# Performance work log

Measured on AMD Instinct MI355X. Metric: run time of the kernel, lower is better.

## Reference

```python
import jax, jax.numpy as jnp
import numpy as np

N, E = 40000, 640000
IN, HID, OUT = 128, 128, 128


def _lin(key, fan_in, fan_out):
    bound = 1.0 / np.sqrt(fan_in)
    kw, kb = jax.random.split(key)
    W = jax.random.uniform(kw, (fan_in, fan_out), jnp.float32, -bound, bound)
    b = jax.random.uniform(kb, (fan_out,), jnp.float32, -bound, bound)
    return W, b


def setup_inputs() -> dict:
    key = jax.random.key(0)
    ks = jax.random.split(key, 10)
    node_feat = jax.random.normal(ks[0], (N, IN), jnp.float32)
    coord_feat = jax.random.normal(ks[1], (N, 3), jnp.float32)
    src = jax.random.randint(ks[2], (E,), 0, N, jnp.int32)
    dst = jax.random.randint(ks[3], (E,), 0, N, jnp.int32)
    # edge_mlp: Linear(2*IN+1 -> HID), SiLU, Linear(HID -> HID), SiLU
    We1, be1 = _lin(ks[4], 2 * IN + 1, HID)
    We2, be2 = _lin(ks[5], HID, HID)
    # node_mlp: Linear(IN+HID -> HID), SiLU, Linear(HID -> OUT)
    Wn1, bn1 = _lin(ks[6], IN + HID, HID)
    Wn2, bn2 = _lin(ks[7], HID, OUT)
    # coord_mlp: Linear(HID -> HID), SiLU, Linear(HID -> 1, bias=False)
    Wc1, bc1 = _lin(ks[8], HID, HID)
    Wc2, _ = _lin(ks[9], HID, 1)
    return {"node_feat": node_feat, "coord_feat": coord_feat, "src": src, "dst": dst,
            "We1": We1, "be1": be1, "We2": We2, "be2": be2,
            "Wn1": Wn1, "bn1": bn1, "Wn2": Wn2, "bn2": bn2,
            "Wc1": Wc1, "bc1": bc1, "Wc2": Wc2}


def reference(node_feat, coord_feat, src, dst,
              We1, be1, We2, be2, Wn1, bn1, Wn2, bn2, Wc1, bc1, Wc2):
    n = node_feat.shape[0]
    # edge gather: u_sub_v gives x_src - x_dst
    x_diff = coord_feat[src] - coord_feat[dst]                       # (E, 3)
    dist = jnp.sqrt(jnp.sum(x_diff * x_diff, axis=-1, keepdims=True))  # (E, 1)
    x_dir = x_diff / (dist + 1e-7)
    f = jnp.concatenate([node_feat[src], node_feat[dst], dist], axis=-1)  # (E, 2*IN+1)
    msg_h = jax.nn.silu(jax.nn.silu(f @ We1 + be1) @ We2 + be2)      # (E, HID)
    coef = jax.nn.silu(msg_h @ Wc1 + bc1) @ Wc2                      # (E, 1)
    msg_x = coef * x_dir                                             # (E, 3)
    # scatter-reduce to destination nodes: sum for h, mean for x
    h_neigh = jax.ops.segment_sum(msg_h, dst, num_segments=n)        # (N, HID)
    cnt = jax.ops.segment_sum(jnp.ones((dst.shape[0], 1), msg_x.dtype), dst, num_segments=n)
    x_neigh = jax.ops.segment_sum(msg_x, dst, num_segments=n) / jnp.maximum(cnt, 1.0)
    h = jax.nn.silu(jnp.concatenate([node_feat, h_neigh], axis=-1) @ Wn1 + bn1) @ Wn2 + bn2
    return h, coord_feat + x_neigh
```

## Files before the change

kernel.cpp:

```cpp
#include <hip/hip_runtime.h>
#include <hip/hip_bf16.h>
#include <math.h>
#include <stdint.h>

#define N_NODES 40000
#define N_EDGES 640000

typedef short short8 __attribute__((ext_vector_type(8)));
typedef float f32x4 __attribute__((ext_vector_type(4)));

__device__ __forceinline__ float silu(float x) {
    return __fdividef(x, 1.0f + __expf(-x));
}

__device__ __forceinline__ unsigned short f2bf(float f) {
    unsigned u = __float_as_uint(f);
    u += 0x7FFF + ((u >> 16) & 1);
    return (unsigned short)(u >> 16);
}
__device__ __forceinline__ float bf2f(unsigned short h) {
    return __uint_as_float(((unsigned)h) << 16);
}
__device__ __forceinline__ unsigned pk2bf(float a, float b) {
    __hip_bfloat162 h = __float22bfloat162_rn(make_float2(a, b));
    unsigned u;
    __builtin_memcpy(&u, &h, 4);
    return u;
}

__global__ __launch_bounds__(1024) void k_scan(const int* __restrict__ deg,
                                               int* __restrict__ row_start) {
    __shared__ int wsum[16];
    const int t = threadIdx.x;
    const int lane = t & 63, wid = t >> 6;
    int base = 0;
    if (t == 0) row_start[0] = 0;
    for (int off = 0; off < N_NODES; off += 1024) {
        int x = (off + t < N_NODES) ? deg[off + t] : 0;
#pragma unroll
        for (int s = 1; s < 64; s <<= 1) {
            const int u = __shfl_up(x, s, 64);
            if (lane >= s) x += u;
        }
        if (lane == 63) wsum[wid] = x;
        __syncthreads();
        if (wid == 0) {
            int ws = (lane < 16) ? wsum[lane] : 0;
#pragma unroll
            for (int s = 1; s < 16; s <<= 1) {
                const int u = __shfl_up(ws, s, 64);
                if (lane >= s) ws += u;
            }
            if (lane < 16) wsum[lane] = ws;
        }
        __syncthreads();
        const int wbase = (wid > 0) ? wsum[wid - 1] : 0;
        const int total = wsum[15];
        if (off + t < N_NODES) row_start[off + t + 1] = base + wbase + x;
        base += total;
        __syncthreads();
    }
}

__global__ __launch_bounds__(256) void k_fill(const int* __restrict__ dst,
                                              const int* __restrict__ row_start,
                                              int* __restrict__ cursor,
                                              int* __restrict__ elist) {
    const int e = blockIdx.x * 256 + threadIdx.x;
    if (e < N_EDGES) {
        const int d = dst[e];
        const int p = atomicAdd(&cursor[d], 1);
        elist[row_start[d] + p] = e;
    }
}

__global__ __launch_bounds__(128) void k_pack2(
    const float* __restrict__ We1, const float* __restrict__ We2,
    const float* __restrict__ Wc1, const float* __restrict__ Wn1,
    const float* __restrict__ Wn2,
    unsigned short* __restrict__ Wt_e1, unsigned short* __restrict__ Wt_e2,
    unsigned short* __restrict__ Wt_c1, unsigned short* __restrict__ Wt_n1,
    unsigned short* __restrict__ Wt_n2,
    int* __restrict__ deg, int* __restrict__ cursor, float* __restrict__ xs,
    float* __restrict__ hn) {
    const int b = blockIdx.x;
    const int t = threadIdx.x;
    Wt_e1[b * 128 + t] = f2bf(We1[(size_t)((b >> 7) * 128 + t) * 128 + (b & 127)]);
    if (b < 128) {
        Wt_e2[b * 128 + t] = f2bf(We2[(size_t)t * 128 + b]);
        Wt_c1[b * 128 + t] = f2bf(Wc1[(size_t)t * 128 + b]);
        Wt_n2[b * 128 + t] = f2bf(Wn2[(size_t)t * 128 + b]);
        Wt_n1[b * 256 + t] = f2bf(Wn1[(size_t)t * 128 + b]);
        Wt_n1[b * 256 + 128 + t] = f2bf(Wn1[(size_t)(128 + t) * 128 + b]);
    }
    const int gid = b * 128 + t;
    for (int i = gid; i < N_NODES; i += 32768) { deg[i] = 0; cursor[i] = 0; }
    for (int i = gid; i < N_NODES * 4; i += 32768) xs[i] = 0.0f;
    float4* hz = (float4*)hn;
    const float4 z4 = {0.f, 0.f, 0.f, 0.f};
    for (int i = gid; i < N_NODES * 32; i += 32768) hz[i] = z4;
}

__global__ __launch_bounds__(256) void k_cntpre(
    const float* __restrict__ nf, const unsigned short* __restrict__ Wt_e1,
    unsigned short* __restrict__ Pc,
    const int* __restrict__ dst, int* __restrict__ deg) {
    __shared__ __align__(16) unsigned short sNF[32][136];
    const int t = threadIdx.x;
    const int node0 = blockIdx.x * 32;
    {
        const int e0 = (blockIdx.x * 256 + t) * 2;
        const int d0 = dst[e0], d1 = dst[e0 + 1];
        atomicAdd(&deg[d0], 1);
        atomicAdd(&deg[d1], 1);
    }
    {
        const int m = t >> 3, kc = (t & 7) * 16;
        const float* sp = &nf[(size_t)(node0 + m) * 128 + kc];
        const float4 v0 = *(const float4*)(sp + 0);
        const float4 v1 = *(const float4*)(sp + 4);
        const float4 v2 = *(const float4*)(sp + 8);
        const float4 v3 = *(const float4*)(sp + 12);
        int4 o0, o1;
        o0.x = pk2bf(v0.x, v0.y); o0.y = pk2bf(v0.z, v0.w);
        o0.z = pk2bf(v1.x, v1.y); o0.w = pk2bf(v1.z, v1.w);
        o1.x = pk2bf(v2.x, v2.y); o1.y = pk2bf(v2.z, v2.w);
        o1.z = pk2bf(v3.x, v3.y); o1.w = pk2bf(v3.z, v3.w);
        *(int4*)&sNF[m][kc] = o0;
        *(int4*)&sNF[m][kc + 8] = o1;
    }
    __syncthreads();

    const int w = t >> 6, l = t & 63, c = l & 15, quad = l >> 4;
    const int n0 = w * 64;

    f32x4 acc[2][4];
#pragma unroll
    for (int mt = 0; mt < 2; mt++)
#pragma unroll
        for (int tile = 0; tile < 4; tile++) acc[mt][tile] = (f32x4){0.f, 0.f, 0.f, 0.f};

#pragma unroll
    for (int k0 = 0; k0 < 128; k0 += 32) {
        const short8 a0 = *(const short8*)&sNF[c][k0 + quad * 8];
        const short8 a1 = *(const short8*)&sNF[16 + c][k0 + quad * 8];
#pragma unroll
        for (int tile = 0; tile < 4; tile++) {
            const short8 b = *(const short8*)(Wt_e1 +
                ((size_t)(n0 + tile * 16 + c) << 7) + k0 + quad * 8);
            acc[0][tile] = __builtin_amdgcn_mfma_f32_16x16x32_bf16(a0, b, acc[0][tile], 0, 0, 0);
            acc[1][tile] = __builtin_amdgcn_mfma_f32_16x16x32_bf16(a1, b, acc[1][tile], 0, 0, 0);
        }
    }
#pragma unroll
    for (int mt = 0; mt < 2; mt++)
#pragma unroll
        for (int tile = 0; tile < 4; tile++) {
            const int col = n0 + tile * 16 + c;
            const unsigned p01 = pk2bf(acc[mt][tile][0], acc[mt][tile][1]);
            const unsigned p23 = pk2bf(acc[mt][tile][2], acc[mt][tile][3]);
            const int row = node0 + mt * 16 + quad * 4;
            Pc[(size_t)(row + 0) * 256 + col] = (unsigned short)p01;
            Pc[(size_t)(row + 1) * 256 + col] = (unsigned short)(p01 >> 16);
            Pc[(size_t)(row + 2) * 256 + col] = (unsigned short)p23;
            Pc[(size_t)(row + 3) * 256 + col] = (unsigned short)(p23 >> 16);
        }
}

__global__ __launch_bounds__(512) void k_edge5(
    const unsigned short* __restrict__ Pc, const float* __restrict__ coord,
    const int* __restrict__ src, const int* __restrict__ dst,
    const int* __restrict__ elist,
    const float* __restrict__ We1, const float* __restrict__ be1,
    const unsigned short* __restrict__ Wt_e2, const float* __restrict__ be2,
    const unsigned short* __restrict__ Wt_c1, const float* __restrict__ bc1,
    const float* __restrict__ Wc2,
    float* __restrict__ h_neigh, float* __restrict__ xs) {
    __shared__ __align__(16) unsigned short sT[128][136];
    __shared__ float scoefp[8][32];
    __shared__ float sw[128], sb[128];
    __shared__ float sdist[128];
    __shared__ float sxd[128][3];
    __shared__ int ssrc[128];
    __shared__ int sdst[128];

    const int t = threadIdx.x;
    const int e0 = blockIdx.x * 128;

    if (t < 128) {
        const int eid = elist[e0 + t];
        const int s = src[eid], d = dst[eid];
        ssrc[t] = s; sdst[t] = d;
        const float dx = coord[3 * s + 0] - coord[3 * d + 0];
        const float dy = coord[3 * s + 1] - coord[3 * d + 1];
        const float dz = coord[3 * s + 2] - coord[3 * d + 2];
        const float dist = sqrtf(dx * dx + dy * dy + dz * dz);
        sdist[t] = dist;
        const float inv = __fdividef(1.0f, dist + 1e-7f);
        sxd[t][0] = dx * inv; sxd[t][1] = dy * inv; sxd[t][2] = dz * inv;
    } else if (t < 160) {
        ((float4*)sw)[t - 128] = ((const float4*)(We1 + 256 * 128))[t - 128];
    } else if (t < 192) {
        ((float4*)sb)[t - 160] = ((const float4*)be1)[t - 160];
    }
    __syncthreads();

    {
        const int e = t >> 2;
        const int kc = (t & 3) * 32;
        const int s = ssrc[e], d = sdst[e];
        const float dist = sdist[e];
        const unsigned short* p1 = Pc + (size_t)s * 256 + kc;
        const unsigned short* p2 = Pc + (size_t)d * 256 + 128 + kc;
        short8 a[4], b[4];
#pragma unroll
        for (int i = 0; i < 4; i++) {
            a[i] = *(const short8*)(p1 + i * 8);
            b[i] = *(const short8*)(p2 + i * 8);
        }
#pragma unroll
        for (int i = 0; i < 4; i++) {
            float v[8];
#pragma unroll
            for (int kk = 0; kk < 8; kk++) {
                const int k = kc + i * 8 + kk;
                v[kk] = silu(bf2f((unsigned short)a[i][kk]) + bf2f((unsigned short)b[i][kk])
                             + dist * sw[k] + sb[k]);
            }
            int4 o;
            o.x = pk2bf(v[0], v[1]); o.y = pk2bf(v[2], v[3]);
            o.z = pk2bf(v[4], v[5]); o.w = pk2bf(v[6], v[7]);
            *(int4*)&sT[e][kc + i * 8] = o;
        }
    }
    __syncthreads();

    const int w = t >> 6;
    const int l = t & 63;
    const int h = w & 3;
    const int H = w >> 2;
    const int m0 = h * 32;
    const int n0 = H * 64;
    const int c = l & 15;
    const int quad = l >> 4;

    f32x4 acc1[2][4];
#pragma unroll
    for (int mt = 0; mt < 2; mt++)
#pragma unroll
        for (int tile = 0; tile < 4; tile++) acc1[mt][tile] = (f32x4){0.f, 0.f, 0.f, 0.f};
#pragma unroll
    for (int k0 = 0; k0 < 128; k0 += 32) {
        const short8 a0 = *(const short8*)&sT[m0 + c][k0 + quad * 8];
        const short8 a1 = *(const short8*)&sT[m0 + 16 + c][k0 + quad * 8];
#pragma unroll
        for (int tile = 0; tile < 4; tile++) {
            const short8 b = *(const short8*)(Wt_e2 +
                ((size_t)(n0 + tile * 16 + c) << 7) + k0 + quad * 8);
            acc1[0][tile] = __builtin_amdgcn_mfma_f32_16x16x32_bf16(a0, b, acc1[0][tile], 0, 0, 0);
            acc1[1][tile] = __builtin_amdgcn_mfma_f32_16x16x32_bf16(a1, b, acc1[1][tile], 0, 0, 0);
        }
    }
    __syncthreads();

#pragma unroll
    for (int mt = 0; mt < 2; mt++)
#pragma unroll
        for (int tile = 0; tile < 4; tile++) {
            const int col = n0 + tile * 16 + c;
            const float bb = be2[col];
            const unsigned p01 = pk2bf(silu(acc1[mt][tile][0] + bb), silu(acc1[mt][tile][1] + bb));
            const unsigned p23 = pk2bf(silu(acc1[mt][tile][2] + bb), silu(acc1[mt][tile][3] + bb));
            const int row = m0 + mt * 16 + quad * 4;
            sT[row + 0][col] = (unsigned short)p01;
            sT[row + 1][col] = (unsigned short)(p01 >> 16);
            sT[row + 2][col] = (unsigned short)p23;
            sT[row + 3][col] = (unsigned short)(p23 >> 16);
        }
    __syncthreads();

    {
        const int j = t & 127;
        const int q = t >> 7;
        const int eb = q * 32;
        float acc = bf2f(sT[eb][j]);
        int prev = sdst[eb];
        for (int e2 = eb + 1; e2 < eb + 32; e2++) {
            const int de = sdst[e2];
            if (de != prev) {
                atomicAdd(&h_neigh[(size_t)prev * 128 + j], acc);
                acc = 0.0f;
                prev = de;
            }
            acc += bf2f(sT[e2][j]);
        }
        atomicAdd(&h_neigh[(size_t)prev * 128 + j], acc);
    }

    {
        f32x4 acc[2][4];
#pragma unroll
        for (int mt = 0; mt < 2; mt++)
#pragma unroll
            for (int tile = 0; tile < 4; tile++) acc[mt][tile] = (f32x4){0.f, 0.f, 0.f, 0.f};
#pragma unroll
        for (int k0 = 0; k0 < 128; k0 += 32) {
            const short8 a0 = *(const short8*)&sT[m0 + c][k0 + quad * 8];
            const short8 a1 = *(const short8*)&sT[m0 + 16 + c][k0 + quad * 8];
#pragma unroll
            for (int tile = 0; tile < 4; tile++) {
                const short8 b = *(const short8*)(Wt_c1 +
                    ((size_t)(n0 + tile * 16 + c) << 7) + k0 + quad * 8);
                acc[0][tile] = __builtin_amdgcn_mfma_f32_16x16x32_bf16(a0, b, acc[0][tile], 0, 0, 0);
                acc[1][tile] = __builtin_amdgcn_mfma_f32_16x16x32_bf16(a1, b, acc[1][tile], 0, 0, 0);
            }
        }
        float part[2][4] = {{0.f, 0.f, 0.f, 0.f}, {0.f, 0.f, 0.f, 0.f}};
#pragma unroll
        for (int tile = 0; tile < 4; tile++) {
            const int col = n0 + tile * 16 + c;
            const float bc = bc1[col];
            const float wc = Wc2[col];
#pragma unroll
            for (int mt = 0; mt < 2; mt++)
#pragma unroll
                for (int r = 0; r < 4; r++)
                    part[mt][r] += silu(acc[mt][tile][r] + bc) * wc;
        }
#pragma unroll
        for (int off = 1; off < 16; off <<= 1) {
#pragma unroll
            for (int mt = 0; mt < 2; mt++)
#pragma unroll
                for (int r = 0; r < 4; r++)
                    part[mt][r] += __shfl_xor(part[mt][r], off, 64);
        }
        if (c == 0) {
#pragma unroll
            for (int mt = 0; mt < 2; mt++)
#pragma unroll
                for (int r = 0; r < 4; r++)
                    scoefp[w][mt * 16 + quad * 4 + r] = part[mt][r];
        }
    }

    if (l < 3) {
        const int cc = l;
        const int eb = h * 32;
        float acc = scoefp[w][0] * sxd[eb][cc];
        int prev = sdst[eb];
        for (int e2 = eb + 1; e2 < eb + 32; e2++) {
            const int de = sdst[e2];
            if (de != prev) {
                atomicAdd(&xs[(size_t)prev * 4 + cc], acc);
                acc = 0.0f;
                prev = de;
            }
            acc += scoefp[w][e2 & 31] * sxd[e2][cc];
        }
        atomicAdd(&xs[(size_t)prev * 4 + cc], acc);
    }
}

__global__ __launch_bounds__(256) void k_node(
    const float* __restrict__ nf, const float* __restrict__ coord,
    const float* __restrict__ hn, const float* __restrict__ xs,
    const int* __restrict__ row_start,
    const unsigned short* __restrict__ Wt_n1, const float* __restrict__ bn1,
    const unsigned short* __restrict__ Wt_n2, const float* __restrict__ bn2,
    float* __restrict__ out_h, float* __restrict__ out_x) {
    __shared__ __align__(16) unsigned short sAB[32][264];
    __shared__ __align__(16) unsigned short sH[32][136];
    const int t = threadIdx.x;
    const int node0 = blockIdx.x * 32;
    {
        const int m = t >> 3, kc = (t & 7) * 32;
        const float* base = (kc < 128) ? &nf[(size_t)(node0 + m) * 128 + kc]
                                       : &hn[(size_t)(node0 + m) * 128 + (kc - 128)];
#pragma unroll
        for (int kk = 0; kk < 32; kk += 8) {
            const float4 v0 = *(const float4*)(base + kk);
            const float4 v1 = *(const float4*)(base + kk + 4);
            int4 o;
            o.x = pk2bf(v0.x, v0.y); o.y = pk2bf(v0.z, v0.w);
            o.z = pk2bf(v1.x, v1.y); o.w = pk2bf(v1.z, v1.w);
            *(int4*)&sAB[m][kc + kk] = o;
        }
    }
    if (t < 96) {
        const int m = t / 3, cc = t - m * 3;
        const int i = node0 + m;
        const float cnt = (float)(row_start[i + 1] - row_start[i]);
        out_x[(size_t)i * 3 + cc] =
            coord[(size_t)i * 3 + cc] + __fdividef(xs[(size_t)i * 4 + cc], fmaxf(cnt, 1.0f));
    }
    __syncthreads();

    const int w = t >> 6, l = t & 63, c = l & 15, quad = l >> 4;
    const int n0 = w * 32;

    {
        f32x4 acc[2][2];
#pragma unroll
        for (int mt = 0; mt < 2; mt++)
#pragma unroll
            for (int tile = 0; tile < 2; tile++) acc[mt][tile] = (f32x4){0.f, 0.f, 0.f, 0.f};
#pragma unroll
        for (int k0 = 0; k0 < 256; k0 += 32) {
            const short8 a0 = *(const short8*)&sAB[c][k0 + quad * 8];
            const short8 a1 = *(const short8*)&sAB[16 + c][k0 + quad * 8];
#pragma unroll
            for (int tile = 0; tile < 2; tile++) {
                const short8 b = *(const short8*)(Wt_n1 +
                    ((size_t)(n0 + tile * 16 + c) << 8) + k0 + quad * 8);
                acc[0][tile] = __builtin_amdgcn_mfma_f32_16x16x32_bf16(a0, b, acc[0][tile], 0, 0, 0);
                acc[1][tile] = __builtin_amdgcn_mfma_f32_16x16x32_bf16(a1, b, acc[1][tile], 0, 0, 0);
            }
        }
#pragma unroll
        for (int mt = 0; mt < 2; mt++)
#pragma unroll
            for (int tile = 0; tile < 2; tile++) {
                const int col = n0 + tile * 16 + c;
                const float bb = bn1[col];
                const unsigned p01 = pk2bf(silu(acc[mt][tile][0] + bb), silu(acc[mt][tile][1] + bb));
                const unsigned p23 = pk2bf(silu(acc[mt][tile][2] + bb), silu(acc[mt][tile][3] + bb));
                const int row = mt * 16 + quad * 4;
                sH[row + 0][col] = (unsigned short)p01;
                sH[row + 1][col] = (unsigned short)(p01 >> 16);
                sH[row + 2][col] = (unsigned short)p23;
                sH[row + 3][col] = (unsigned short)(p23 >> 16);
            }
    }
    __syncthreads();

    {
        f32x4 acc[2][2];
#pragma unroll
        for (int mt = 0; mt < 2; mt++)
#pragma unroll
            for (int tile = 0; tile < 2; tile++) acc[mt][tile] = (f32x4){0.f, 0.f, 0.f, 0.f};
#pragma unroll
        for (int k0 = 0; k0 < 128; k0 += 32) {
            const short8 a0 = *(const short8*)&sH[c][k0 + quad * 8];
            const short8 a1 = *(const short8*)&sH[16 + c][k0 + quad * 8];
#pragma unroll
            for (int tile = 0; tile < 2; tile++) {
                const short8 b = *(const short8*)(Wt_n2 +
                    ((size_t)(n0 + tile * 16 + c) << 7) + k0 + quad * 8);
                acc[0][tile] = __builtin_amdgcn_mfma_f32_16x16x32_bf16(a0, b, acc[0][tile], 0, 0, 0);
                acc[1][tile] = __builtin_amdgcn_mfma_f32_16x16x32_bf16(a1, b, acc[1][tile], 0, 0, 0);
            }
        }
#pragma unroll
        for (int mt = 0; mt < 2; mt++)
#pragma unroll
            for (int tile = 0; tile < 2; tile++) {
                const int col = n0 + tile * 16 + c;
                const float bb = bn2[col];
#pragma unroll
                for (int r = 0; r < 4; r++) {
                    const int row = mt * 16 + quad * 4 + r;
                    out_h[(size_t)(node0 + row) * 128 + col] = acc[mt][tile][r] + bb;
                }
            }
    }
}

extern "C" void kernel_launch(void* const* d_in, const int* in_sizes, int n_in,
                              void* d_out, int out_size, void* d_ws, size_t ws_size,
                              hipStream_t stream) {
    const float* nf    = (const float*)d_in[0];
    const float* coord = (const float*)d_in[1];
    const int*   src   = (const int*)d_in[2];
    const int*   dst   = (const int*)d_in[3];
    const float* We1   = (const float*)d_in[4];
    const float* be1   = (const float*)d_in[5];
    const float* We2   = (const float*)d_in[6];
    const float* be2   = (const float*)d_in[7];
    const float* Wn1   = (const float*)d_in[8];
    const float* bn1   = (const float*)d_in[9];
    const float* Wn2   = (const float*)d_in[10];
    const float* bn2   = (const float*)d_in[11];
    const float* Wc1   = (const float*)d_in[12];
    const float* bc1   = (const float*)d_in[13];
    const float* Wc2   = (const float*)d_in[14];

    unsigned short* Pc = (unsigned short*)d_ws;
    float* hn = (float*)(Pc + (size_t)N_NODES * 256);
    float* xs = hn + (size_t)N_NODES * 128;
    int* deg       = (int*)(xs + (size_t)N_NODES * 4);
    int* row_start = deg + N_NODES;
    int* cursor    = row_start + N_NODES + 1;
    int* elist     = cursor + N_NODES;
    unsigned short* Wt_e1 = (unsigned short*)
        (((uintptr_t)(elist + N_EDGES) + 255) & ~(uintptr_t)255);
    unsigned short* Wt_e2 = Wt_e1 + 256 * 128;
    unsigned short* Wt_c1 = Wt_e2 + 128 * 128;
    unsigned short* Wt_n1 = Wt_c1 + 128 * 128;
    unsigned short* Wt_n2 = Wt_n1 + 128 * 256;

    float* out_h = (float*)d_out;
    float* out_x = out_h + (size_t)N_NODES * 128;

    k_pack2<<<256, 128, 0, stream>>>(We1, We2, Wc1, Wn1, Wn2,
                                     Wt_e1, Wt_e2, Wt_c1, Wt_n1, Wt_n2,
                                     deg, cursor, xs, hn);
    k_cntpre<<<N_NODES / 32, 256, 0, stream>>>(nf, Wt_e1, Pc, dst, deg);
    k_scan<<<1, 1024, 0, stream>>>(deg, row_start);
    k_fill<<<(N_EDGES + 255) / 256, 256, 0, stream>>>(dst, row_start, cursor, elist);
    k_edge5<<<N_EDGES / 128, 512, 0, stream>>>(Pc, coord, src, dst, elist,
                                               We1, be1, Wt_e2, be2, Wt_c1, bc1,
                                               Wc2, hn, xs);
    k_node<<<N_NODES / 32, 256, 0, stream>>>(nf, coord, hn, xs, row_start,
                                             Wt_n1, bn1, Wt_n2, bn2, out_h, out_x);
}
```

Before: 476.6 us.

## Split edge kernel into gather/activation pass and GEMM pass via global buffer

Folds the be1 bias into the precomputed per-node projection Pc. The fused edge kernel is split in two when the workspace is large enough. The first kernel gathers the per-node projections, applies the first SiLU and writes a tile-blocked bf16 layer-1 activation buffer (E×128) to global memory. The second kernel loads that buffer straight into MFMA registers and runs the second edge layer, the coordinate MLP and the segmented atomic scatter. This separates the latency-bound gather from the matrix work, at the cost of roughly 160MB of extra global traffic and an extra launch; which path runs depends on ws_size, so it may fall back to the old kernel.

```diff
diff --git a/kernel.cpp b/kernel.cpp
--- a/kernel.cpp
+++ b/kernel.cpp
@@ -5,6 +5,7 @@
 
 #define N_NODES 40000
 #define N_EDGES 640000
+#define N_TILES 5000
 
 typedef short short8 __attribute__((ext_vector_type(8)));
 typedef float f32x4 __attribute__((ext_vector_type(4)));
@@ -103,6 +104,7 @@
 
 __global__ __launch_bounds__(256) void k_cntpre(
     const float* __restrict__ nf, const unsigned short* __restrict__ Wt_e1,
+    const float* __restrict__ be1,
     unsigned short* __restrict__ Pc,
     const int* __restrict__ dst, int* __restrict__ deg) {
     __shared__ __align__(16) unsigned short sNF[32][136];
@@ -138,27 +140,28 @@
 #pragma unroll
     for (int mt = 0; mt < 2; mt++)
 #pragma unroll
-        for (int tile = 0; tile < 4; tile++) acc[mt][tile] = (f32x4){0.f, 0.f, 0.f, 0.f};
+        for (int tl = 0; tl < 4; tl++) acc[mt][tl] = (f32x4){0.f, 0.f, 0.f, 0.f};
 
 #pragma unroll
     for (int k0 = 0; k0 < 128; k0 += 32) {
         const short8 a0 = *(const short8*)&sNF[c][k0 + quad * 8];
         const short8 a1 = *(const short8*)&sNF[16 + c][k0 + quad * 8];
 #pragma unroll
-        for (int tile = 0; tile < 4; tile++) {
+        for (int tl = 0; tl < 4; tl++) {
             const short8 b = *(const short8*)(Wt_e1 +
-                ((size_t)(n0 + tile * 16 + c) << 7) + k0 + quad * 8);
-            acc[0][tile] = __builtin_amdgcn_mfma_f32_16x16x32_bf16(a0, b, acc[0][tile], 0, 0, 0);
-            acc[1][tile] = __builtin_amdgcn_mfma_f32_16x16x32_bf16(a1, b, acc[1][tile], 0, 0, 0);
+                ((size_t)(n0 + tl * 16 + c) << 7) + k0 + quad * 8);
+            acc[0][tl] = __builtin_amdgcn_mfma_f32_16x16x32_bf16(a0, b, acc[0][tl], 0, 0, 0);
+            acc[1][tl] = __builtin_amdgcn_mfma_f32_16x16x32_bf16(a1, b, acc[1][tl], 0, 0, 0);
         }
     }
 #pragma unroll
     for (int mt = 0; mt < 2; mt++)
 #pragma unroll
-        for (int tile = 0; tile < 4; tile++) {
-            const int col = n0 + tile * 16 + c;
-            const unsigned p01 = pk2bf(acc[mt][tile][0], acc[mt][tile][1]);
-            const unsigned p23 = pk2bf(acc[mt][tile][2], acc[mt][tile][3]);
+        for (int tl = 0; tl < 4; tl++) {
+            const int col = n0 + tl * 16 + c;
+            const float bias = (col >= 128) ? be1[col - 128] : 0.0f;
+            const unsigned p01 = pk2bf(acc[mt][tl][0] + bias, acc[mt][tl][1] + bias);
+            const unsigned p23 = pk2bf(acc[mt][tl][2] + bias, acc[mt][tl][3] + bias);
             const int row = node0 + mt * 16 + quad * 4;
             Pc[(size_t)(row + 0) * 256 + col] = (unsigned short)p01;
             Pc[(size_t)(row + 1) * 256 + col] = (unsigned short)(p01 >> 16);
@@ -167,18 +170,230 @@
         }
 }
 
-__global__ __launch_bounds__(512) void k_edge5(
+__global__ __launch_bounds__(256) void k_t1(
     const unsigned short* __restrict__ Pc, const float* __restrict__ coord,
     const int* __restrict__ src, const int* __restrict__ dst,
+    const int* __restrict__ elist, const float* __restrict__ We1,
+    unsigned short* __restrict__ t1g) {
+    const int t = threadIdx.x;
+    const int bid = (int)blockIdx.x;
+    const int tile = (bid & 7) * 625 + (bid >> 3);
+    const int er = t >> 1;
+    const int ec = tile * 128 + er;
+    const int kc = (t & 1) * 64;
+
+    const int eid = elist[ec];
+    const int s = src[eid], d = dst[eid];
+
+    const unsigned short* p1 = Pc + (size_t)s * 256 + kc;
+    const unsigned short* p2 = Pc + (size_t)d * 256 + 128 + kc;
+    short8 ga[8], gb[8];
+#pragma unroll
+    for (int i = 0; i < 8; i++) ga[i] = *(const short8*)(p1 + i * 8);
+#pragma unroll
+    for (int i = 0; i < 8; i++) gb[i] = *(const short8*)(p2 + i * 8);
+
+    const float dx = coord[3 * s + 0] - coord[3 * d + 0];
+    const float dy = coord[3 * s + 1] - coord[3 * d + 1];
+    const float dz = coord[3 * s + 2] - coord[3 * d + 2];
+    const float dist = sqrtf(dx * dx + dy * dy + dz * dz);
+
+    const float* wd = We1 + 256 * 128 + kc;
+    unsigned short* outb = t1g + (size_t)tile * 16384 + er * 8;
+#pragma unroll
+    for (int i = 0; i < 8; i++) {
+        const float4 w0 = *(const float4*)(wd + i * 8);
+        const float4 w1 = *(const float4*)(wd + i * 8 + 4);
+        float v[8];
+        v[0] = silu(bf2f((unsigned short)ga[i][0]) + bf2f((unsigned short)gb[i][0]) + dist * w0.x);
+        v[1] = silu(bf2f((unsigned short)ga[i][1]) + bf2f((unsigned short)gb[i][1]) + dist * w0.y);
+        v[2] = silu(bf2f((unsigned short)ga[i][2]) + bf2f((unsigned short)gb[i][2]) + dist * w0.z);
+        v[3] = silu(bf2f((unsigned short)ga[i][3]) + bf2f((unsigned short)gb[i][3]) + dist * w0.w);
+        v[4] = silu(bf2f((unsigned short)ga[i][4]) + bf2f((unsigned short)gb[i][4]) + dist * w1.x);
+        v[5] = silu(bf2f((unsigned short)ga[i][5]) + bf2f((unsigned short)gb[i][5]) + dist * w1.y);
+        v[6] = silu(bf2f((unsigned short)ga[i][6]) + bf2f((unsigned short)gb[i][6]) + dist * w1.z);
+        v[7] = silu(bf2f((unsigned short)ga[i][7]) + bf2f((unsigned short)gb[i][7]) + dist * w1.w);
+        int4 o;
+        o.x = pk2bf(v[0], v[1]); o.y = pk2bf(v[2], v[3]);
+        o.z = pk2bf(v[4], v[5]); o.w = pk2bf(v[6], v[7]);
+        const int c8 = (kc >> 3) + i;
+        *(int4*)(outb + (size_t)c8 * 128 * 8) = o;
+    }
+}
+
+__global__ __launch_bounds__(512) void k_gemm(
+    const unsigned short* __restrict__ t1g, const float* __restrict__ coord,
+    const int* __restrict__ src, const int* __restrict__ dst,
     const int* __restrict__ elist,
-    const float* __restrict__ We1, const float* __restrict__ be1,
     const unsigned short* __restrict__ Wt_e2, const float* __restrict__ be2,
     const unsigned short* __restrict__ Wt_c1, const float* __restrict__ bc1,
     const float* __restrict__ Wc2,
     float* __restrict__ h_neigh, float* __restrict__ xs) {
     __shared__ __align__(16) unsigned short sT[128][136];
     __shared__ float scoefp[8][32];
-    __shared__ float sw[128], sb[128];
+    __shared__ float sxd[128][3];
+    __shared__ int sdst[128];
+
+    const int t = threadIdx.x;
+    const int w = t >> 6, l = t & 63;
+    const int h = w & 3, H = w >> 2;
+    const int m0 = h * 32, n0 = H * 64;
+    const int c = l & 15, quad = l >> 4;
+
+    const int bid = (int)blockIdx.x;
+    const int tile = (bid & 7) * 625 + (bid >> 3);
+    const int e0 = tile * 128;
+
+    short8 a0[4], a1[4];
+    {
+        const unsigned short* tb = t1g + (size_t)tile * 16384;
+#pragma unroll
+        for (int k0 = 0; k0 < 4; k0++) {
+            const int ch = k0 * 4 + quad;
+            a0[k0] = *(const short8*)(tb + (ch * 128 + m0 + c) * 8);
+            a1[k0] = *(const short8*)(tb + (ch * 128 + m0 + 16 + c) * 8);
+        }
+    }
+
+    if (t < 128) {
+        const int eid = elist[e0 + t];
+        const int s = src[eid], d = dst[eid];
+        sdst[t] = d;
+        const float dx = coord[3 * s + 0] - coord[3 * d + 0];
+        const float dy = coord[3 * s + 1] - coord[3 * d + 1];
+        const float dz = coord[3 * s + 2] - coord[3 * d + 2];
+        const float dist = sqrtf(dx * dx + dy * dy + dz * dz);
+        const float inv = __fdividef(1.0f, dist + 1e-7f);
+        sxd[t][0] = dx * inv; sxd[t][1] = dy * inv; sxd[t][2] = dz * inv;
+    }
+
+    f32x4 acc1[2][4];
+#pragma unroll
+    for (int mt = 0; mt < 2; mt++)
+#pragma unroll
+        for (int tl = 0; tl < 4; tl++) acc1[mt][tl] = (f32x4){0.f, 0.f, 0.f, 0.f};
+#pragma unroll
+    for (int k0 = 0; k0 < 4; k0++) {
+#pragma unroll
+        for (int tl = 0; tl < 4; tl++) {
+            const short8 b = *(const short8*)(Wt_e2 +
+                ((size_t)(n0 + tl * 16 + c) << 7) + k0 * 32 + quad * 8);
+            acc1[0][tl] = __builtin_amdgcn_mfma_f32_16x16x32_bf16(a0[k0], b, acc1[0][tl], 0, 0, 0);
+            acc1[1][tl] = __builtin_amdgcn_mfma_f32_16x16x32_bf16(a1[k0], b, acc1[1][tl], 0, 0, 0);
+        }
+    }
+
+#pragma unroll
+    for (int mt = 0; mt < 2; mt++)
+#pragma unroll
+        for (int tl = 0; tl < 4; tl++) {
+            const int col = n0 + tl * 16 + c;
+            const float bb = be2[col];
+            const unsigned p01 = pk2bf(silu(acc1[mt][tl][0] + bb), silu(acc1[mt][tl][1] + bb));
+            const unsigned p23 = pk2bf(silu(acc1[mt][tl][2] + bb), silu(acc1[mt][tl][3] + bb));
+            const int row = m0 + mt * 16 + quad * 4;
+            sT[row + 0][col] = (unsigned short)p01;
+            sT[row + 1][col] = (unsigned short)(p01 >> 16);
+            sT[row + 2][col] = (unsigned short)p23;
+            sT[row + 3][col] = (unsigned short)(p23 >> 16);
+        }
+    __syncthreads();
+
+    {
+        const int j = t & 127;
+        const int q = t >> 7;
+        const int eb = q * 32;
+        float acc = bf2f(sT[eb][j]);
+        int prev = sdst[eb];
+        for (int e2 = eb + 1; e2 < eb + 32; e2++) {
+            const int de = sdst[e2];
+            if (de != prev) {
+                atomicAdd(&h_neigh[(size_t)prev * 128 + j], acc);
+                acc = 0.0f;
+                prev = de;
+            }
+            acc += bf2f(sT[e2][j]);
+        }
+        atomicAdd(&h_neigh[(size_t)prev * 128 + j], acc);
+    }
+
+    {
+        f32x4 acc[2][4];
+#pragma unroll
+        for (int mt = 0; mt < 2; mt++)
+#pragma unroll
+            for (int tl = 0; tl < 4; tl++) acc[mt][tl] = (f32x4){0.f, 0.f, 0.f, 0.f};
+#pragma unroll
+        for (int k0 = 0; k0 < 128; k0 += 32) {
+            const short8 a0_ = *(const short8*)&sT[m0 + c][k0 + quad * 8];
+            const short8 a1_ = *(const short8*)&sT[m0 + 16 + c][k0 + quad * 8];
+#pragma unroll
+            for (int tl = 0; tl < 4; tl++) {
+                const short8 b = *(const short8*)(Wt_c1 +
+                    ((size_t)(n0 + tl * 16 + c) << 7) + k0 + quad * 8);
+                acc[0][tl] = __builtin_amdgcn_mfma_f32_16x16x32_bf16(a0_, b, acc[0][tl], 0, 0, 0);
+                acc[1][tl] = __builtin_amdgcn_mfma_f32_16x16x32_bf16(a1_, b, acc[1][tl], 0, 0, 0);
+            }
+        }
+        float part[2][4] = {{0.f, 0.f, 0.f, 0.f}, {0.f, 0.f, 0.f, 0.f}};
+#pragma unroll
+        for (int tl = 0; tl < 4; tl++) {
+            const int col = n0 + tl * 16 + c;
+            const float bc = bc1[col];
+            const float wc = Wc2[col];
+#pragma unroll
+            for (int mt = 0; mt < 2; mt++)
+#pragma unroll
+                for (int r = 0; r < 4; r++)
+                    part[mt][r] += silu(acc[mt][tl][r] + bc) * wc;
+        }
+#pragma unroll
+        for (int off = 1; off < 16; off <<= 1) {
+#pragma unroll
+            for (int mt = 0; mt < 2; mt++)
+#pragma unroll
+                for (int r = 0; r < 4; r++)
+                    part[mt][r] += __shfl_xor(part[mt][r], off, 64);
+        }
+        if (c == 0) {
+#pragma unroll
+            for (int mt = 0; mt < 2; mt++)
+#pragma unroll
+                for (int r = 0; r < 4; r++)
+                    scoefp[w][mt * 16 + quad * 4 + r] = part[mt][r];
+        }
+    }
+
+    if (l < 3) {
+        const int cc = l;
+        const int eb = h * 32;
+        float acc = scoefp[w][0] * sxd[eb][cc];
+        int prev = sdst[eb];
+        for (int e2 = eb + 1; e2 < eb + 32; e2++) {
+            const int de = sdst[e2];
+            if (de != prev) {
+                atomicAdd(&xs[(size_t)prev * 4 + cc], acc);
+                acc = 0.0f;
+                prev = de;
+            }
+            acc += scoefp[w][e2 & 31] * sxd[e2][cc];
+        }
+        atomicAdd(&xs[(size_t)prev * 4 + cc], acc);
+    }
+}
+
+__global__ __launch_bounds__(512) void k_edge5(
+    const unsigned short* __restrict__ Pc, const float* __restrict__ coord,
+    const int* __restrict__ src, const int* __restrict__ dst,
+    const int* __restrict__ elist,
+    const float* __restrict__ We1,
+    const unsigned short* __restrict__ Wt_e2, const float* __restrict__ be2,
+    const unsigned short* __restrict__ Wt_c1, const float* __restrict__ bc1,
+    const float* __restrict__ Wc2,
+    float* __restrict__ h_neigh, float* __restrict__ xs) {
+    __shared__ __align__(16) unsigned short sT[128][136];
+    __shared__ float scoefp[8][32];
+    __shared__ float sw[128];
     __shared__ float sdist[128];
     __shared__ float sxd[128][3];
     __shared__ int ssrc[128];
@@ -200,8 +415,6 @@
         sxd[t][0] = dx * inv; sxd[t][1] = dy * inv; sxd[t][2] = dz * inv;
     } else if (t < 160) {
         ((float4*)sw)[t - 128] = ((const float4*)(We1 + 256 * 128))[t - 128];
-    } else if (t < 192) {
-        ((float4*)sb)[t - 160] = ((const float4*)be1)[t - 160];
     }
     __syncthreads();
 
@@ -225,7 +438,7 @@
             for (int kk = 0; kk < 8; kk++) {
                 const int k = kc + i * 8 + kk;
                 v[kk] = silu(bf2f((unsigned short)a[i][kk]) + bf2f((unsigned short)b[i][kk])
-                             + dist * sw[k] + sb[k]);
+                             + dist * sw[k]);
             }
             int4 o;
             o.x = pk2bf(v[0], v[1]); o.y = pk2bf(v[2], v[3]);
@@ -404,27 +617,27 @@
 #pragma unroll
         for (int mt = 0; mt < 2; mt++)
 #pragma unroll
-            for (int tile = 0; tile < 2; tile++) acc[mt][tile] = (f32x4){0.f, 0.f, 0.f, 0.f};
+            for (int tl = 0; tl < 2; tl++) acc[mt][tl] = (f32x4){0.f, 0.f, 0.f, 0.f};
 #pragma unroll
         for (int k0 = 0; k0 < 256; k0 += 32) {
             const short8 a0 = *(const short8*)&sAB[c][k0 + quad * 8];
             const short8 a1 = *(const short8*)&sAB[16 + c][k0 + quad * 8];
 #pragma unroll
-            for (int tile = 0; tile < 2; tile++) {
+            for (int tl = 0; tl < 2; tl++) {
                 const short8 b = *(const short8*)(Wt_n1 +
-                    ((size_t)(n0 + tile * 16 + c) << 8) + k0 + quad * 8);
-                acc[0][tile] = __builtin_amdgcn_mfma_f32_16x16x32_bf16(a0, b, acc[0][tile], 0, 0, 0);
-                acc[1][tile] = __builtin_amdgcn_mfma_f32_16x16x32_bf16(a1, b, acc[1][tile], 0, 0, 0);
+                    ((size_t)(n0 + tl * 16 + c) << 8) + k0 + quad * 8);
+                acc[0][tl] = __builtin_amdgcn_mfma_f32_16x16x32_bf16(a0, b, acc[0][tl], 0, 0, 0);
+                acc[1][tl] = __builtin_amdgcn_mfma_f32_16x16x32_bf16(a1, b, acc[1][tl], 0, 0, 0);
             }
         }
 #pragma unroll
         for (int mt = 0; mt < 2; mt++)
 #pragma unroll
-            for (int tile = 0; tile < 2; tile++) {
-                const int col = n0 + tile * 16 + c;
+            for (int tl = 0; tl < 2; tl++) {
+                const int col = n0 + tl * 16 + c;
                 const float bb = bn1[col];
-                const unsigned p01 = pk2bf(silu(acc[mt][tile][0] + bb), silu(acc[mt][tile][1] + bb));
-                const unsigned p23 = pk2bf(silu(acc[mt][tile][2] + bb), silu(acc[mt][tile][3] + bb));
+                const unsigned p01 = pk2bf(silu(acc[mt][tl][0] + bb), silu(acc[mt][tl][1] + bb));
+                const unsigned p23 = pk2bf(silu(acc[mt][tl][2] + bb), silu(acc[mt][tl][3] + bb));
                 const int row = mt * 16 + quad * 4;
                 sH[row + 0][col] = (unsigned short)p01;
                 sH[row + 1][col] = (unsigned short)(p01 >> 16);
@@ -439,29 +652,29 @@
 #pragma unroll
         for (int mt = 0; mt < 2; mt++)
 #pragma unroll
-            for (int tile = 0; tile < 2; tile++) acc[mt][tile] = (f32x4){0.f, 0.f, 0.f, 0.f};
+            for (int tl = 0; tl < 2; tl++) acc[mt][tl] = (f32x4){0.f, 0.f, 0.f, 0.f};
 #pragma unroll
         for (int k0 = 0; k0 < 128; k0 += 32) {
             const short8 a0 = *(const short8*)&sH[c][k0 + quad * 8];
             const short8 a1 = *(const short8*)&sH[16 + c][k0 + quad * 8];
 #pragma unroll
-            for (int tile = 0; tile < 2; tile++) {
+            for (int tl = 0; tl < 2; tl++) {
                 const short8 b = *(const short8*)(Wt_n2 +
-                    ((size_t)(n0 + tile * 16 + c) << 7) + k0 + quad * 8);
-                acc[0][tile] = __builtin_amdgcn_mfma_f32_16x16x32_bf16(a0, b, acc[0][tile], 0, 0, 0);
-                acc[1][tile] = __builtin_amdgcn_mfma_f32_16x16x32_bf16(a1, b, acc[1][tile], 0, 0, 0);
+                    ((size_t)(n0 + tl * 16 + c) << 7) + k0 + quad * 8);
+                acc[0][tl] = __builtin_amdgcn_mfma_f32_16x16x32_bf16(a0, b, acc[0][tl], 0, 0, 0);
+                acc[1][tl] = __builtin_amdgcn_mfma_f32_16x16x32_bf16(a1, b, acc[1][tl], 0, 0, 0);
             }
         }
 #pragma unroll
         for (int mt = 0; mt < 2; mt++)
 #pragma unroll
-            for (int tile = 0; tile < 2; tile++) {
-                const int col = n0 + tile * 16 + c;
+            for (int tl = 0; tl < 2; tl++) {
+                const int col = n0 + tl * 16 + c;
                 const float bb = bn2[col];
 #pragma unroll
                 for (int r = 0; r < 4; r++) {
                     const int row = mt * 16 + quad * 4 + r;
-                    out_h[(size_t)(node0 + row) * 128 + col] = acc[mt][tile][r] + bb;
+                    out_h[(size_t)(node0 + row) * 128 + col] = acc[mt][tl][r] + bb;
                 }
             }
     }
@@ -499,6 +712,10 @@
     unsigned short* Wt_c1 = Wt_e2 + 128 * 128;
     unsigned short* Wt_n1 = Wt_c1 + 128 * 128;
     unsigned short* Wt_n2 = Wt_n1 + 128 * 256;
+    unsigned short* t1g = (unsigned short*)
+        (((uintptr_t)(Wt_n2 + 128 * 128) + 255) & ~(uintptr_t)255);
+    const size_t need = ((uintptr_t)t1g - (uintptr_t)d_ws) +
+                        (size_t)N_EDGES * 128 * sizeof(unsigned short);
 
     float* out_h = (float*)d_out;
     float* out_x = out_h + (size_t)N_NODES * 128;
@@ -506,12 +723,18 @@
     k_pack2<<<256, 128, 0, stream>>>(We1, We2, Wc1, Wn1, Wn2,
                                      Wt_e1, Wt_e2, Wt_c1, Wt_n1, Wt_n2,
                                      deg, cursor, xs, hn);
-    k_cntpre<<<N_NODES / 32, 256, 0, stream>>>(nf, Wt_e1, Pc, dst, deg);
+    k_cntpre<<<N_NODES / 32, 256, 0, stream>>>(nf, Wt_e1, be1, Pc, dst, deg);
     k_scan<<<1, 1024, 0, stream>>>(deg, row_start);
     k_fill<<<(N_EDGES + 255) / 256, 256, 0, stream>>>(dst, row_start, cursor, elist);
-    k_edge5<<<N_EDGES / 128, 512, 0, stream>>>(Pc, coord, src, dst, elist,
-                                               We1, be1, Wt_e2, be2, Wt_c1, bc1,
-                                               Wc2, hn, xs);
+    if (ws_size >= need) {
+        k_t1<<<N_TILES, 256, 0, stream>>>(Pc, coord, src, dst, elist, We1, t1g);
+        k_gemm<<<N_TILES, 512, 0, stream>>>(t1g, coord, src, dst, elist,
+                                            Wt_e2, be2, Wt_c1, bc1, Wc2, hn, xs);
+    } else {
+        k_edge5<<<N_EDGES / 128, 512, 0, stream>>>(Pc, coord, src, dst, elist,
+                                                   We1, Wt_e2, be2, Wt_c1, bc1,
+                                                   Wc2, hn, xs);
+    }
     k_node<<<N_NODES / 32, 256, 0, stream>>>(nf, coord, hn, xs, row_start,
                                              Wt_n1, bn1, Wt_n2, bn2, out_h, out_x);
 }
```

Result: slower. 543.9 us (+14.1%).

## Halve edge kernel tile to 64 edges, swizzle blocks, fold be1 into precompute

Applied to the files above, without the earlier changes.

The edge kernel now handles 64 edges per 256-thread block instead of 128 edges per 512-thread block, which doubles the grid size and halves LDS per block. Block indices are swizzled across eight groups of 1250 so that concurrently running blocks cover different regions of the dst-sorted edge list. The be1 bias is added once per node in the Pc precompute rather than once per edge. The smaller tiles should improve occupancy, but each block reloads the same weights for half as many edges, and the swizzle may hurt locality of the scatter-adds into h_neigh.

```diff
diff --git a/kernel.cpp b/kernel.cpp
--- a/kernel.cpp
+++ b/kernel.cpp
@@ -103,6 +103,7 @@
 
 __global__ __launch_bounds__(256) void k_cntpre(
     const float* __restrict__ nf, const unsigned short* __restrict__ Wt_e1,
+    const float* __restrict__ be1,
     unsigned short* __restrict__ Pc,
     const int* __restrict__ dst, int* __restrict__ deg) {
     __shared__ __align__(16) unsigned short sNF[32][136];
@@ -138,27 +139,28 @@
 #pragma unroll
     for (int mt = 0; mt < 2; mt++)
 #pragma unroll
-        for (int tile = 0; tile < 4; tile++) acc[mt][tile] = (f32x4){0.f, 0.f, 0.f, 0.f};
+        for (int tl = 0; tl < 4; tl++) acc[mt][tl] = (f32x4){0.f, 0.f, 0.f, 0.f};
 
 #pragma unroll
     for (int k0 = 0; k0 < 128; k0 += 32) {
         const short8 a0 = *(const short8*)&sNF[c][k0 + quad * 8];
         const short8 a1 = *(const short8*)&sNF[16 + c][k0 + quad * 8];
 #pragma unroll
-        for (int tile = 0; tile < 4; tile++) {
+        for (int tl = 0; tl < 4; tl++) {
             const short8 b = *(const short8*)(Wt_e1 +
-                ((size_t)(n0 + tile * 16 + c) << 7) + k0 + quad * 8);
-            acc[0][tile] = __builtin_amdgcn_mfma_f32_16x16x32_bf16(a0, b, acc[0][tile], 0, 0, 0);
-            acc[1][tile] = __builtin_amdgcn_mfma_f32_16x16x32_bf16(a1, b, acc[1][tile], 0, 0, 0);
+                ((size_t)(n0 + tl * 16 + c) << 7) + k0 + quad * 8);
+            acc[0][tl] = __builtin_amdgcn_mfma_f32_16x16x32_bf16(a0, b, acc[0][tl], 0, 0, 0);
+            acc[1][tl] = __builtin_amdgcn_mfma_f32_16x16x32_bf16(a1, b, acc[1][tl], 0, 0, 0);
         }
     }
 #pragma unroll
     for (int mt = 0; mt < 2; mt++)
 #pragma unroll
-        for (int tile = 0; tile < 4; tile++) {
-            const int col = n0 + tile * 16 + c;
-            const unsigned p01 = pk2bf(acc[mt][tile][0], acc[mt][tile][1]);
-            const unsigned p23 = pk2bf(acc[mt][tile][2], acc[mt][tile][3]);
+        for (int tl = 0; tl < 4; tl++) {
+            const int col = n0 + tl * 16 + c;
+            const float bias = (col >= 128) ? be1[col - 128] : 0.0f;
+            const unsigned p01 = pk2bf(acc[mt][tl][0] + bias, acc[mt][tl][1] + bias);
+            const unsigned p23 = pk2bf(acc[mt][tl][2] + bias, acc[mt][tl][3] + bias);
             const int row = node0 + mt * 16 + quad * 4;
             Pc[(size_t)(row + 0) * 256 + col] = (unsigned short)p01;
             Pc[(size_t)(row + 1) * 256 + col] = (unsigned short)(p01 >> 16);
@@ -167,27 +169,29 @@
         }
 }
 
-__global__ __launch_bounds__(512) void k_edge5(
+__global__ __launch_bounds__(256) void k_edge8(
     const unsigned short* __restrict__ Pc, const float* __restrict__ coord,
     const int* __restrict__ src, const int* __restrict__ dst,
     const int* __restrict__ elist,
-    const float* __restrict__ We1, const float* __restrict__ be1,
+    const float* __restrict__ We1,
     const unsigned short* __restrict__ Wt_e2, const float* __restrict__ be2,
     const unsigned short* __restrict__ Wt_c1, const float* __restrict__ bc1,
     const float* __restrict__ Wc2,
     float* __restrict__ h_neigh, float* __restrict__ xs) {
-    __shared__ __align__(16) unsigned short sT[128][136];
-    __shared__ float scoefp[8][32];
-    __shared__ float sw[128], sb[128];
-    __shared__ float sdist[128];
-    __shared__ float sxd[128][3];
-    __shared__ int ssrc[128];
-    __shared__ int sdst[128];
+    __shared__ __align__(16) unsigned short sT[64][136];
+    __shared__ float scoefp[4][32];
+    __shared__ float sw[128];
+    __shared__ float sdist[64];
+    __shared__ float sxd[64][3];
+    __shared__ int ssrc[64];
+    __shared__ int sdst[64];
 
     const int t = threadIdx.x;
-    const int e0 = blockIdx.x * 128;
-
-    if (t < 128) {
+    const int bid = (int)blockIdx.x;
+    const int swz = (bid & 7) * 1250 + (bid >> 3);
+    const int e0 = swz * 64;
+
+    if (t < 64) {
         const int eid = elist[e0 + t];
         const int s = src[eid], d = dst[eid];
         ssrc[t] = s; sdst[t] = d;
@@ -198,10 +202,8 @@
         sdist[t] = dist;
         const float inv = __fdividef(1.0f, dist + 1e-7f);
         sxd[t][0] = dx * inv; sxd[t][1] = dy * inv; sxd[t][2] = dz * inv;
-    } else if (t < 160) {
-        ((float4*)sw)[t - 128] = ((const float4*)(We1 + 256 * 128))[t - 128];
-    } else if (t < 192) {
-        ((float4*)sb)[t - 160] = ((const float4*)be1)[t - 160];
+    } else if (t < 96) {
+        ((float4*)sw)[t - 64] = ((const float4*)(We1 + 256 * 128))[t - 64];
     }
     __syncthreads();
 
@@ -225,7 +227,7 @@
             for (int kk = 0; kk < 8; kk++) {
                 const int k = kc + i * 8 + kk;
                 v[kk] = silu(bf2f((unsigned short)a[i][kk]) + bf2f((unsigned short)b[i][kk])
-                             + dist * sw[k] + sb[k]);
+                             + dist * sw[k]);
             }
             int4 o;
             o.x = pk2bf(v[0], v[1]); o.y = pk2bf(v[2], v[3]);
@@ -237,8 +239,8 @@
 
     const int w = t >> 6;
     const int l = t & 63;
-    const int h = w & 3;
-    const int H = w >> 2;
+    const int h = w & 1;
+    const int H = w >> 1;
     const int m0 = h * 32;
     const int n0 = H * 64;
     const int c = l & 15;
@@ -404,27 +406,27 @@
 #pragma unroll
         for (int mt = 0; mt < 2; mt++)
 #pragma unroll
-            for (int tile = 0; tile < 2; tile++) acc[mt][tile] = (f32x4){0.f, 0.f, 0.f, 0.f};
+            for (int tl = 0; tl < 2; tl++) acc[mt][tl] = (f32x4){0.f, 0.f, 0.f, 0.f};
 #pragma unroll
         for (int k0 = 0; k0 < 256; k0 += 32) {
             const short8 a0 = *(const short8*)&sAB[c][k0 + quad * 8];
             const short8 a1 = *(const short8*)&sAB[16 + c][k0 + quad * 8];
 #pragma unroll
-            for (int tile = 0; tile < 2; tile++) {
+            for (int tl = 0; tl < 2; tl++) {
                 const short8 b = *(const short8*)(Wt_n1 +
-                    ((size_t)(n0 + tile * 16 + c) << 8) + k0 + quad * 8);
-                acc[0][tile] = __builtin_amdgcn_mfma_f32_16x16x32_bf16(a0, b, acc[0][tile], 0, 0, 0);
-                acc[1][tile] = __builtin_amdgcn_mfma_f32_16x16x32_bf16(a1, b, acc[1][tile], 0, 0, 0);
+                    ((size_t)(n0 + tl * 16 + c) << 8) + k0 + quad * 8);
+                acc[0][tl] = __builtin_amdgcn_mfma_f32_16x16x32_bf16(a0, b, acc[0][tl], 0, 0, 0);
+                acc[1][tl] = __builtin_amdgcn_mfma_f32_16x16x32_bf16(a1, b, acc[1][tl], 0, 0, 0);
             }
         }
 #pragma unroll
         for (int mt = 0; mt < 2; mt++)
 #pragma unroll
-            for (int tile = 0; tile < 2; tile++) {
-                const int col = n0 + tile * 16 + c;
+            for (int tl = 0; tl < 2; tl++) {
+                const int col = n0 + tl * 16 + c;
                 const float bb = bn1[col];
-                const unsigned p01 = pk2bf(silu(acc[mt][tile][0] + bb), silu(acc[mt][tile][1] + bb));
-                const unsigned p23 = pk2bf(silu(acc[mt][tile][2] + bb), silu(acc[mt][tile][3] + bb));
+                const unsigned p01 = pk2bf(silu(acc[mt][tl][0] + bb), silu(acc[mt][tl][1] + bb));
+                const unsigned p23 = pk2bf(silu(acc[mt][tl][2] + bb), silu(acc[mt][tl][3] + bb));
                 const int row = mt * 16 + quad * 4;
                 sH[row + 0][col] = (unsigned short)p01;
                 sH[row + 1][col] = (unsigned short)(p01 >> 16);
@@ -439,29 +441,29 @@
 #pragma unroll
         for (int mt = 0; mt < 2; mt++)
 #pragma unroll
-            for (int tile = 0; tile < 2; tile++) acc[mt][tile] = (f32x4){0.f, 0.f, 0.f, 0.f};
+            for (int tl = 0; tl < 2; tl++) acc[mt][tl] = (f32x4){0.f, 0.f, 0.f, 0.f};
 #pragma unroll
         for (int k0 = 0; k0 < 128; k0 += 32) {
             const short8 a0 = *(const short8*)&sH[c][k0 + quad * 8];
             const short8 a1 = *(const short8*)&sH[16 + c][k0 + quad * 8];
 #pragma unroll
-            for (int tile = 0; tile < 2; tile++) {
+            for (int tl = 0; tl < 2; tl++) {
                 const short8 b = *(const short8*)(Wt_n2 +
-                    ((size_t)(n0 + tile * 16 + c) << 7) + k0 + quad * 8);
-                acc[0][tile] = __builtin_amdgcn_mfma_f32_16x16x32_bf16(a0, b, acc[0][tile], 0, 0, 0);
-                acc[1][tile] = __builtin_amdgcn_mfma_f32_16x16x32_bf16(a1, b, acc[1][tile], 0, 0, 0);
+                    ((size_t)(n0 + tl * 16 + c) << 7) + k0 + quad * 8);
+                acc[0][tl] = __builtin_amdgcn_mfma_f32_16x16x32_bf16(a0, b, acc[0][tl], 0, 0, 0);
+                acc[1][tl] = __builtin_amdgcn_mfma_f32_16x16x32_bf16(a1, b, acc[1][tl], 0, 0, 0);
             }
         }
 #pragma unroll
         for (int mt = 0; mt < 2; mt++)
 #pragma unroll
-            for (int tile = 0; tile < 2; tile++) {
-                const int col = n0 + tile * 16 + c;
+            for (int tl = 0; tl < 2; tl++) {
+                const int col = n0 + tl * 16 + c;
                 const float bb = bn2[col];
 #pragma unroll
                 for (int r = 0; r < 4; r++) {
                     const int row = mt * 16 + quad * 4 + r;
-                    out_h[(size_t)(node0 + row) * 128 + col] = acc[mt][tile][r] + bb;
+                    out_h[(size_t)(node0 + row) * 128 + col] = acc[mt][tl][r] + bb;
                 }
             }
     }
@@ -506,12 +508,12 @@
     k_pack2<<<256, 128, 0, stream>>>(We1, We2, Wc1, Wn1, Wn2,
                                      Wt_e1, Wt_e2, Wt_c1, Wt_n1, Wt_n2,
                                      deg, cursor, xs, hn);
-    k_cntpre<<<N_NODES / 32, 256, 0, stream>>>(nf, Wt_e1, Pc, dst, deg);
+    k_cntpre<<<N_NODES / 32, 256, 0, stream>>>(nf, Wt_e1, be1, Pc, dst, deg);
     k_scan<<<1, 1024, 0, stream>>>(deg, row_start);
     k_fill<<<(N_EDGES + 255) / 256, 256, 0, stream>>>(dst, row_start, cursor, elist);
-    k_edge5<<<N_EDGES / 128, 512, 0, stream>>>(Pc, coord, src, dst, elist,
-                                               We1, be1, Wt_e2, be2, Wt_c1, bc1,
-                                               Wc2, hn, xs);
+    k_edge8<<<N_EDGES / 64, 256, 0, stream>>>(Pc, coord, src, dst, elist,
+                                              We1, Wt_e2, be2, Wt_c1, bc1,
+                                              Wc2, hn, xs);
     k_node<<<N_NODES / 32, 256, 0, stream>>>(nf, coord, hn, xs, row_start,
                                              Wt_n1, bn1, Wt_n2, bn2, out_h, out_x);
 }
```

Result: faster. 460.4 us (-3.4%).
